# Kernel optimization log

Hardware: AMD Instinct MI355X
Metric: run time of the kernel (lower is better)

## Reference

```python
import jax, jax.numpy as jnp
import numpy as np
import math

B, LQ, LK, D, H = 4, 1024, 1024, 1024, 16
DK = D // H
SCALE = 1.0 / math.sqrt(DK)
NEG_INF = -1.0e9


def setup_inputs() -> dict:
    key = jax.random.key(0)
    ks = jax.random.split(key, 18)
    w = lambda k: (jax.random.normal(k, (D, D), dtype=jnp.float32) * 0.02)
    b = lambda k: (jax.random.normal(k, (D,), dtype=jnp.float32) * 0.02)
    mask = jax.random.randint(ks[4], (B, 1, LK), 0, 2).astype(jnp.int32)
    mask = mask.at[..., 0].set(1)  # ensure at least one valid key per row
    return {
        "query": jax.random.normal(ks[0], (B, LQ, D), dtype=jnp.float32),
        "key": jax.random.normal(ks[1], (B, LK, D), dtype=jnp.float32),
        "value": jax.random.normal(ks[2], (B, LK, D), dtype=jnp.float32),
        "weak_rela": jax.random.normal(ks[3], (B, LK, D), dtype=jnp.float32),
        "mask": mask,
        "Wq": w(ks[5]), "bq": b(ks[6]),
        "Wk": w(ks[7]), "bk": b(ks[8]),
        "Wv": w(ks[9]), "bv": b(ks[10]),
        "Wrk": w(ks[11]), "brk": b(ks[12]),
        "Wrv": w(ks[13]), "brv": b(ks[14]),
        "Wo": w(ks[15]), "bo": b(ks[16]),
    }


def _proj(x, W, bias):
    # x: [B, L, D] -> [B, H, L, DK]; torch Linear: y = x @ W.T + b
    y = x @ W.T + bias
    Bn, L, _ = y.shape
    return y.reshape(Bn, L, H, DK).transpose(0, 2, 1, 3)


def reference(query, key, value, weak_rela, mask,
              Wq, bq, Wk, bk, Wv, bv, Wrk, brk, Wrv, brv, Wo, bo):
    q = _proj(query, Wq, bq)        # [B,H,LQ,DK]
    k = _proj(key, Wk, bk)          # [B,H,LK,DK]
    v = _proj(value, Wv, bv)        # [B,H,LK,DK]
    rk = _proj(weak_rela, Wrk, brk) # [B,H,LK,DK]
    rv = _proj(weak_rela, Wrv, brv) # [B,H,LK,DK]

    qk = jnp.einsum('bhqd,bhkd->bhqk', q, k) * SCALE
    qr = jnp.einsum('bhqd,bhkd->bhqk', q, rk) * SCALE

    m = (mask[:, None, :, :] == 0)  # [B,1,1,LK] broadcast over heads/queries
    qk = jnp.where(m, NEG_INF, qk)
    qr = jnp.where(m, NEG_INF, qr)

    p_vis = jax.nn.softmax(qk, axis=-1)
    p_rel = jax.nn.softmax(qr, axis=-1)

    x = (jnp.einsum('bhqk,bhkd->bhqd', p_vis, v)
         + jnp.einsum('bhqk,bhkd->bhqd', p_rel, rv))  # [B,H,LQ,DK]
    x = x.transpose(0, 2, 1, 3).reshape(query.shape[0], -1, H * DK)
    return x @ Wo.T + bo
```

## Files before the change

kernel.cpp:

```cpp
#include <hip/hip_runtime.h>
#include <stdint.h>

#define NB 4
#define NH 16
#define DKH 64
#define DMODEL 1024
#define SEQ 1024
#define SCALE 0.125f
#define NEG_INF -1.0e9f
#define K2E 0.18033688011112042f

typedef __bf16 bf16_t;
typedef __bf16 bf16x8 __attribute__((ext_vector_type(8)));
typedef __bf16 bf16x4v __attribute__((ext_vector_type(4)));
typedef float f32x4 __attribute__((ext_vector_type(4)));

typedef const uint32_t __attribute__((address_space(1)))* gas_ptr;
typedef uint32_t __attribute__((address_space(3)))* las_ptr;

__device__ __forceinline__ void gload_lds16(const void* g, void* l) {
  __builtin_amdgcn_global_load_lds((gas_ptr)g, (las_ptr)l, 16, 0, 0);
}


__global__ void cvt_multi(const float* __restrict__ i0, const float* __restrict__ i1,
                          const float* __restrict__ i2, const float* __restrict__ i3,
                          const float* __restrict__ i4, const float* __restrict__ i5,
                          bf16_t* o0, bf16_t* o1, bf16_t* o2, bf16_t* o3, bf16_t* o4, bf16_t* o5,
                          int n) {
  const int t = blockIdx.y;
  const float* in = (t == 0) ? i0 : (t == 1) ? i1 : (t == 2) ? i2 : (t == 3) ? i3 : (t == 4) ? i4 : i5;
  bf16_t* out = (t == 0) ? o0 : (t == 1) ? o1 : (t == 2) ? o2 : (t == 3) ? o3 : (t == 4) ? o4 : o5;
  const int idx = (blockIdx.x * 256 + threadIdx.x) * 4;
  if (idx >= n) return;
  const float4 v = *(const float4*)(in + idx);
  bf16x4v p;
  p[0] = (bf16_t)v.x; p[1] = (bf16_t)v.y; p[2] = (bf16_t)v.z; p[3] = (bf16_t)v.w;
  *(bf16x4v*)(out + idx) = p;
}

#define NXE ((size_t)NB * SEQ * DMODEL)
#define NWE ((size_t)DMODEL * DMODEL)

template<int MODE>
__device__ __forceinline__ void gemm128_body(
    const bf16_t* __restrict__ A, const bf16_t* __restrict__ W,
    const float* __restrict__ bias, void* __restrict__ outp,
    int m0, int n0, bf16_t* As, bf16_t* Bs) {
  const int tid = threadIdx.x;
  const int lane = tid & 63;
  const int w = tid >> 6;
  const int wm = w >> 1, wn = w & 1;
  const int g = lane >> 4, c = lane & 15;
  const int lrow = lane >> 3;
  const int lcol = ((lane & 7) * 8) ^ ((lane >> 3) << 3);
  const int sc = (c & 7) << 3;

  f32x4 acc[4][4] = {};

  for (int kt = 0; kt < DMODEL; kt += 64) {
#pragma unroll
    for (int p = 0; p < 4; ++p) {
      const int row = w * 32 + p * 8;
      gload_lds16(A + (size_t)(m0 + row + lrow) * DMODEL + kt + lcol, &As[row * 64]);
      gload_lds16(W + (size_t)(n0 + row + lrow) * DMODEL + kt + lcol, &Bs[row * 64]);
    }
    __syncthreads();
    bf16x8 af[4][2], bfr[4][2];
#pragma unroll
    for (int i = 0; i < 4; ++i)
#pragma unroll
      for (int kk = 0; kk < 2; ++kk) {
        af[i][kk]  = *(const bf16x8*)&As[(wm * 64 + i * 16 + c) * 64 + ((kk * 32 + g * 8) ^ sc)];
        bfr[i][kk] = *(const bf16x8*)&Bs[(wn * 64 + i * 16 + c) * 64 + ((kk * 32 + g * 8) ^ sc)];
      }
#pragma unroll
    for (int i = 0; i < 4; ++i)
#pragma unroll
      for (int j = 0; j < 4; ++j) {
        acc[i][j] = __builtin_amdgcn_mfma_f32_16x16x32_bf16(af[i][0], bfr[j][0], acc[i][j], 0, 0, 0);
        acc[i][j] = __builtin_amdgcn_mfma_f32_16x16x32_bf16(af[i][1], bfr[j][1], acc[i][j], 0, 0, 0);
      }
    __syncthreads();
  }

  float bv4[4];
#pragma unroll
  for (int j = 0; j < 4; ++j) bv4[j] = bias[n0 + wn * 64 + j * 16 + c];

#pragma unroll
  for (int i = 0; i < 4; ++i) {
    const int mrow = m0 + wm * 64 + i * 16 + g * 4;
    const int b_ = mrow >> 10, l_ = mrow & 1023;
#pragma unroll
    for (int j = 0; j < 4; ++j) {
      const int n = n0 + wn * 64 + j * 16 + c;
      if (MODE == 2) {
        float* o = (float*)outp;
#pragma unroll
        for (int r = 0; r < 4; ++r)
          o[(size_t)(mrow + r) * DMODEL + n] = acc[i][j][r] + bv4[j];
      } else if (MODE == 0) {
        bf16_t* o = (bf16_t*)outp;
        const int h_ = n >> 6, dk_ = n & 63;
#pragma unroll
        for (int r = 0; r < 4; ++r)
          o[((size_t)(b_ * NH + h_) * SEQ + l_ + r) * DKH + dk_] =
              (bf16_t)(acc[i][j][r] + bv4[j]);
      } else {
        bf16_t* o = (bf16_t*)outp;
        const int h_ = n >> 6, dk_ = n & 63;
        bf16x4v pk;
#pragma unroll
        for (int r = 0; r < 4; ++r) pk[r] = (bf16_t)(acc[i][j][r] + bv4[j]);
        *(bf16x4v*)&o[((size_t)(b_ * NH + h_) * DKH + dk_) * SEQ + l_] = pk;
      }
    }
  }
}

__global__ void __launch_bounds__(256, 2)
proj_gemm(const bf16_t* __restrict__ Xbase, const bf16_t* __restrict__ Wbase,
          bf16_t* __restrict__ Obase,
          const float* __restrict__ b0, const float* __restrict__ b1,
          const float* __restrict__ b2, const float* __restrict__ b3,
          const float* __restrict__ b4) {
  __shared__ bf16_t As[128 * 64];
  __shared__ bf16_t Bs[128 * 64];
  const int bid = blockIdx.x;
  const int lid = (bid & 7) * 160 + (bid >> 3);
  const int seg = lid >> 8;
  const int rr = lid & 255;
  const int m0 = (rr >> 3) * 128, n0 = (rr & 7) * 128;

  const bf16_t* A = Xbase + (size_t)((seg < 3) ? seg : 3) * NXE;
  const bf16_t* W = Wbase + (size_t)seg * NWE;
  const int ooff = (seg == 0) ? 0 : (seg == 1) ? 1 : (seg == 2) ? 3 : (seg == 3) ? 2 : 4;
  bf16_t* out = Obase + (size_t)ooff * NXE;
  const float* bias = (seg == 0) ? b0 : (seg == 1) ? b1 : (seg == 2) ? b2 : (seg == 3) ? b3 : b4;

  if (seg == 2 || seg == 4) gemm128_body<1>(A, W, bias, out, m0, n0, As, Bs);
  else                      gemm128_body<0>(A, W, bias, out, m0, n0, As, Bs);
}

__global__ void __launch_bounds__(256, 2)
out_gemm(const bf16_t* __restrict__ A, const bf16_t* __restrict__ W,
         const float* __restrict__ bias, float* __restrict__ out) {
  __shared__ bf16_t As[128 * 64];
  __shared__ bf16_t Bs[128 * 64];
  const int bid = blockIdx.x;
  const int lid = (bid & 7) * 32 + (bid >> 3);
  const int m0 = (lid >> 3) * 128, n0 = (lid & 7) * 128;
  gemm128_body<2>(A, W, bias, out, m0, n0, As, Bs);
}

__device__ __forceinline__ void attn_step(
    const bf16_t* __restrict__ Kt, const bf16_t* __restrict__ Vt,
    bf16_t* __restrict__ Pw, const bf16x8 (&qf)[2][2], const int4 (&mk)[4],
    float (&m_s)[2], float (&l_s)[2], f32x4 (&o_s)[2][4], int lane) {
  const int g = lane >> 4, c = lane & 15;
  const int sc = (c & 7) << 3;

  f32x4 s[2][4];
  {
    bf16x8 kfr[4][2];
#pragma unroll
    for (int f = 0; f < 4; ++f) {
      kfr[f][0] = *(const bf16x8*)&Kt[(f * 16 + c) * 64 + ((g * 8) ^ sc)];
      kfr[f][1] = *(const bf16x8*)&Kt[(f * 16 + c) * 64 + ((32 + g * 8) ^ sc)];
    }
#pragma unroll
    for (int i = 0; i < 2; ++i)
#pragma unroll
      for (int f = 0; f < 4; ++f) {
        f32x4 a = {0.f, 0.f, 0.f, 0.f};
        a = __builtin_amdgcn_mfma_f32_16x16x32_bf16(kfr[f][0], qf[i][0], a, 0, 0, 0);
        a = __builtin_amdgcn_mfma_f32_16x16x32_bf16(kfr[f][1], qf[i][1], a, 0, 0, 0);
        s[i][f] = a;
      }
  }

#pragma unroll
  for (int i = 0; i < 2; ++i)
#pragma unroll
    for (int f = 0; f < 4; ++f) {
      const int4 m4 = mk[f];
      s[i][f][0] = (m4.x == 0) ? NEG_INF : s[i][f][0] * K2E;
      s[i][f][1] = (m4.y == 0) ? NEG_INF : s[i][f][1] * K2E;
      s[i][f][2] = (m4.z == 0) ? NEG_INF : s[i][f][2] * K2E;
      s[i][f][3] = (m4.w == 0) ? NEG_INF : s[i][f][3] * K2E;
    }

#pragma unroll
  for (int i = 0; i < 2; ++i) {
    float tm = fmaxf(fmaxf(s[i][0][0], s[i][0][1]), fmaxf(s[i][0][2], s[i][0][3]));
#pragma unroll
    for (int f = 1; f < 4; ++f)
      tm = fmaxf(tm, fmaxf(fmaxf(s[i][f][0], s[i][f][1]), fmaxf(s[i][f][2], s[i][f][3])));
    tm = fmaxf(tm, __shfl_xor(tm, 16));
    tm = fmaxf(tm, __shfl_xor(tm, 32));
    const float mnew = fmaxf(m_s[i], tm);
    const float sf = __builtin_amdgcn_exp2f(m_s[i] - mnew);
    m_s[i] = mnew;
    float pf = 0.f;
#pragma unroll
    for (int f = 0; f < 4; ++f) {
      bf16x4v pk;
#pragma unroll
      for (int r = 0; r < 4; ++r) {
        const float p = __builtin_amdgcn_exp2f(s[i][f][r] - mnew);
        pf += p;
        pk[r] = (bf16_t)p;
      }
      *(bf16x4v*)&Pw[i * 1024 + c * 64 + ((f * 16 + g * 4) ^ sc)] = pk;
    }
    l_s[i] = l_s[i] * sf + pf;
#pragma unroll
    for (int jd = 0; jd < 4; ++jd)
#pragma unroll
      for (int r = 0; r < 4; ++r) o_s[i][jd][r] *= sf;
  }

  bf16x8 pa[2][2];
#pragma unroll
  for (int i = 0; i < 2; ++i) {
    pa[i][0] = *(const bf16x8*)&Pw[i * 1024 + c * 64 + ((g * 8) ^ sc)];
    pa[i][1] = *(const bf16x8*)&Pw[i * 1024 + c * 64 + ((32 + g * 8) ^ sc)];
  }
#pragma unroll
  for (int jd = 0; jd < 4; ++jd) {
    const bf16x8 v0 = *(const bf16x8*)&Vt[(jd * 16 + c) * 64 + ((g * 8) ^ sc)];
    const bf16x8 v1 = *(const bf16x8*)&Vt[(jd * 16 + c) * 64 + ((32 + g * 8) ^ sc)];
#pragma unroll
    for (int i = 0; i < 2; ++i) {
      o_s[i][jd] = __builtin_amdgcn_mfma_f32_16x16x32_bf16(v0, pa[i][0], o_s[i][jd], 0, 0, 0);
      o_s[i][jd] = __builtin_amdgcn_mfma_f32_16x16x32_bf16(v1, pa[i][1], o_s[i][jd], 0, 0, 0);
    }
  }
}

__global__ void __launch_bounds__(256, 2)
attn_kernel(const bf16_t* __restrict__ q, const bf16_t* __restrict__ k,
            const bf16_t* __restrict__ rk, const bf16_t* __restrict__ vT,
            const bf16_t* __restrict__ rvT, const int* __restrict__ mask,
            bf16_t* __restrict__ x) {
  __shared__ bf16_t Ks[64 * 64], RKs[64 * 64], Vs[64 * 64], RVs[64 * 64];
  __shared__ bf16_t Ps[4][2][16 * 64];

  const int tid = threadIdx.x;
  const int lane = tid & 63;
  const int w = tid >> 6;
  const int g = lane >> 4, c = lane & 15;
  const int bid = blockIdx.x;
  const int lid = (bid & 7) * 64 + (bid >> 3);
  const int qt = lid & 7;
  const int bh = lid >> 3;
  const int b = bh >> 4, h = bh & 15;
  const int q0 = qt * 128;

  const bf16_t* qp = q + (size_t)bh * SEQ * DKH;
  const bf16_t* kp = k + (size_t)bh * SEQ * DKH;
  const bf16_t* rkp = rk + (size_t)bh * SEQ * DKH;
  const bf16_t* vp = vT + (size_t)bh * DKH * SEQ;
  const bf16_t* rvp = rvT + (size_t)bh * DKH * SEQ;
  const int* mp = mask + b * SEQ;
  const int lrow = lane >> 3;
  const int lcol = ((lane & 7) * 8) ^ ((lane >> 3) << 3);

  bf16x8 qf[2][2];
#pragma unroll
  for (int i = 0; i < 2; ++i)
#pragma unroll
    for (int kk = 0; kk < 2; ++kk)
      qf[i][kk] = *(const bf16x8*)(qp + (size_t)(q0 + w * 32 + i * 16 + c) * DKH + kk * 32 + g * 8);

  f32x4 ov[2][4] = {}, orl[2][4] = {};
  float mv[2] = {NEG_INF, NEG_INF}, mr[2] = {NEG_INF, NEG_INF};
  float lv[2] = {0.f, 0.f}, lr[2] = {0.f, 0.f};

  for (int t = 0; t < 16; ++t) {
    const int kv0 = t * 64;
    if (t) __syncthreads();
#pragma unroll
    for (int p = 0; p < 2; ++p) {
      const int row = w * 16 + p * 8;
      gload_lds16(kp  + (size_t)(kv0 + row + lrow) * DKH + lcol, &Ks[row * 64]);
      gload_lds16(rkp + (size_t)(kv0 + row + lrow) * DKH + lcol, &RKs[row * 64]);
      gload_lds16(vp  + (size_t)(row + lrow) * SEQ + kv0 + lcol, &Vs[row * 64]);
      gload_lds16(rvp + (size_t)(row + lrow) * SEQ + kv0 + lcol, &RVs[row * 64]);
    }
    __syncthreads();

    int4 mk4[4];
#pragma unroll
    for (int f = 0; f < 4; ++f) mk4[f] = *(const int4*)&mp[kv0 + f * 16 + g * 4];

    attn_step(Ks,  Vs,  &Ps[w][0][0], qf, mk4, mv, lv, ov,  lane);
    attn_step(RKs, RVs, &Ps[w][0][0], qf, mk4, mr, lr, orl, lane);
  }

#pragma unroll
  for (int i = 0; i < 2; ++i) {
    lv[i] += __shfl_xor(lv[i], 16); lv[i] += __shfl_xor(lv[i], 32);
    lr[i] += __shfl_xor(lr[i], 16); lr[i] += __shfl_xor(lr[i], 32);
  }

  bf16_t* xb = x + (size_t)b * SEQ * DMODEL + (size_t)h * DKH;
#pragma unroll
  for (int i = 0; i < 2; ++i) {
    const float rlv = 1.0f / lv[i], rlr = 1.0f / lr[i];
    const int qrow = q0 + w * 32 + i * 16 + c;
#pragma unroll
    for (int jd = 0; jd < 4; ++jd) {
      bf16x4v pk;
#pragma unroll
      for (int r = 0; r < 4; ++r)
        pk[r] = (bf16_t)(ov[i][jd][r] * rlv + orl[i][jd][r] * rlr);
      *(bf16x4v*)&xb[(size_t)qrow * DMODEL + jd * 16 + g * 4] = pk;
    }
  }
}

extern "C" void kernel_launch(void* const* d_in, const int* in_sizes, int n_in,
                              void* d_out, int out_size, void* d_ws, size_t ws_size,
                              hipStream_t stream) {
  (void)in_sizes; (void)n_in; (void)out_size; (void)ws_size;
  const float* query = (const float*)d_in[0];
  const float* key_  = (const float*)d_in[1];
  const float* value = (const float*)d_in[2];
  const float* weak  = (const float*)d_in[3];
  const int*   mask  = (const int*)d_in[4];
  const float* Wq  = (const float*)d_in[5];  const float* bq  = (const float*)d_in[6];
  const float* Wk  = (const float*)d_in[7];  const float* bk  = (const float*)d_in[8];
  const float* Wv  = (const float*)d_in[9];  const float* bv  = (const float*)d_in[10];
  const float* Wrk = (const float*)d_in[11]; const float* brk = (const float*)d_in[12];
  const float* Wrv = (const float*)d_in[13]; const float* brv = (const float*)d_in[14];
  const float* Wo  = (const float*)d_in[15]; const float* bo  = (const float*)d_in[16];

  char* ws = (char*)d_ws;
  size_t off = 0;
  auto alloc = [&](size_t bytes) {
    void* p = ws + off;
    off += (bytes + 255) & ~(size_t)255;
    return p;
  };
  const size_t SZ_X = NXE * sizeof(bf16_t);
  const size_t SZ_W = NWE * sizeof(bf16_t);

  bf16_t* Xq = (bf16_t*)alloc(SZ_X);
  bf16_t* Xk = (bf16_t*)alloc(SZ_X);
  bf16_t* Xv = (bf16_t*)alloc(SZ_X);
  bf16_t* Xr = (bf16_t*)alloc(SZ_X);
  bf16_t* Wqb  = (bf16_t*)alloc(SZ_W);
  bf16_t* Wkb  = (bf16_t*)alloc(SZ_W);
  bf16_t* Wvb  = (bf16_t*)alloc(SZ_W);
  bf16_t* Wrkb = (bf16_t*)alloc(SZ_W);
  bf16_t* Wrvb = (bf16_t*)alloc(SZ_W);
  bf16_t* Wob  = (bf16_t*)alloc(SZ_W);
  bf16_t* qh   = (bf16_t*)alloc(SZ_X);
  bf16_t* kh   = (bf16_t*)alloc(SZ_X);
  bf16_t* rkh  = (bf16_t*)alloc(SZ_X);
  bf16_t* vTh  = (bf16_t*)alloc(SZ_X);
  bf16_t* rvTh = (bf16_t*)alloc(SZ_X);
  bf16_t* xh   = (bf16_t*)alloc(SZ_X);
  (void)Xk; (void)Xv; (void)Xr; (void)Wkb; (void)Wvb; (void)Wrkb; (void)Wrvb;
  (void)kh; (void)rkh; (void)vTh; (void)rvTh;

  cvt_multi<<<dim3(4096, 4), 256, 0, stream>>>(query, key_, value, weak, nullptr, nullptr,
                                               Xq, Xk, Xv, Xr, nullptr, nullptr,
                                               NB * SEQ * DMODEL);
  cvt_multi<<<dim3(1024, 6), 256, 0, stream>>>(Wq, Wk, Wv, Wrk, Wrv, Wo,
                                               Wqb, Wkb, Wvb, Wrkb, Wrvb, Wob,
                                               DMODEL * DMODEL);

  proj_gemm<<<dim3(1280), 256, 0, stream>>>(Xq, Wqb, qh, bq, bk, bv, brk, brv);

  attn_kernel<<<dim3(512), 256, 0, stream>>>(qh, kh, rkh, vTh, rvTh, mask, xh);

  out_gemm<<<dim3(256), 256, 0, stream>>>(xh, Wob, bo, (float*)d_out);
}
```

Measured before the change: 170.4 us.

## Split attention into separate visual and relation branches across blocks, merge afterwards

Each attention block now handles only one of the two softmax branches (visual or relation), doubling the grid to 1024 blocks and halving per-block LDS and register state. Occupancy hint rises to 3 blocks per CU. Each branch writes normalized fp32 partial outputs into reused workspace buffers, and a new merge kernel sums them and converts to bf16 for the output GEMM. The trade is more parallelism against extra global traffic: fp32 intermediates written and read back, plus one more launch.

```diff
diff --git a/kernel.cpp b/kernel.cpp
--- a/kernel.cpp
+++ b/kernel.cpp
@@ -39,6 +39,18 @@
   *(bf16x4v*)(out + idx) = p;
 }
 
+__global__ void merge_x(const float* __restrict__ xv, const float* __restrict__ xr,
+                        bf16_t* __restrict__ xh, int n) {
+  const int idx = (blockIdx.x * 256 + threadIdx.x) * 4;
+  if (idx >= n) return;
+  const float4 a = *(const float4*)(xv + idx);
+  const float4 b = *(const float4*)(xr + idx);
+  bf16x4v p;
+  p[0] = (bf16_t)(a.x + b.x); p[1] = (bf16_t)(a.y + b.y);
+  p[2] = (bf16_t)(a.z + b.z); p[3] = (bf16_t)(a.w + b.w);
+  *(bf16x4v*)(xh + idx) = p;
+}
+
 #define NXE ((size_t)NB * SEQ * DMODEL)
 #define NWE ((size_t)DMODEL * DMODEL)
 
@@ -154,115 +166,32 @@
   gemm128_body<2>(A, W, bias, out, m0, n0, As, Bs);
 }
 
-__device__ __forceinline__ void attn_step(
-    const bf16_t* __restrict__ Kt, const bf16_t* __restrict__ Vt,
-    bf16_t* __restrict__ Pw, const bf16x8 (&qf)[2][2], const int4 (&mk)[4],
-    float (&m_s)[2], float (&l_s)[2], f32x4 (&o_s)[2][4], int lane) {
-  const int g = lane >> 4, c = lane & 15;
-  const int sc = (c & 7) << 3;
-
-  f32x4 s[2][4];
-  {
-    bf16x8 kfr[4][2];
-#pragma unroll
-    for (int f = 0; f < 4; ++f) {
-      kfr[f][0] = *(const bf16x8*)&Kt[(f * 16 + c) * 64 + ((g * 8) ^ sc)];
-      kfr[f][1] = *(const bf16x8*)&Kt[(f * 16 + c) * 64 + ((32 + g * 8) ^ sc)];
-    }
-#pragma unroll
-    for (int i = 0; i < 2; ++i)
-#pragma unroll
-      for (int f = 0; f < 4; ++f) {
-        f32x4 a = {0.f, 0.f, 0.f, 0.f};
-        a = __builtin_amdgcn_mfma_f32_16x16x32_bf16(kfr[f][0], qf[i][0], a, 0, 0, 0);
-        a = __builtin_amdgcn_mfma_f32_16x16x32_bf16(kfr[f][1], qf[i][1], a, 0, 0, 0);
-        s[i][f] = a;
-      }
-  }
-
-#pragma unroll
-  for (int i = 0; i < 2; ++i)
-#pragma unroll
-    for (int f = 0; f < 4; ++f) {
-      const int4 m4 = mk[f];
-      s[i][f][0] = (m4.x == 0) ? NEG_INF : s[i][f][0] * K2E;
-      s[i][f][1] = (m4.y == 0) ? NEG_INF : s[i][f][1] * K2E;
-      s[i][f][2] = (m4.z == 0) ? NEG_INF : s[i][f][2] * K2E;
-      s[i][f][3] = (m4.w == 0) ? NEG_INF : s[i][f][3] * K2E;
-    }
-
-#pragma unroll
-  for (int i = 0; i < 2; ++i) {
-    float tm = fmaxf(fmaxf(s[i][0][0], s[i][0][1]), fmaxf(s[i][0][2], s[i][0][3]));
-#pragma unroll
-    for (int f = 1; f < 4; ++f)
-      tm = fmaxf(tm, fmaxf(fmaxf(s[i][f][0], s[i][f][1]), fmaxf(s[i][f][2], s[i][f][3])));
-    tm = fmaxf(tm, __shfl_xor(tm, 16));
-    tm = fmaxf(tm, __shfl_xor(tm, 32));
-    const float mnew = fmaxf(m_s[i], tm);
-    const float sf = __builtin_amdgcn_exp2f(m_s[i] - mnew);
-    m_s[i] = mnew;
-    float pf = 0.f;
-#pragma unroll
-    for (int f = 0; f < 4; ++f) {
-      bf16x4v pk;
-#pragma unroll
-      for (int r = 0; r < 4; ++r) {
-        const float p = __builtin_amdgcn_exp2f(s[i][f][r] - mnew);
-        pf += p;
-        pk[r] = (bf16_t)p;
-      }
-      *(bf16x4v*)&Pw[i * 1024 + c * 64 + ((f * 16 + g * 4) ^ sc)] = pk;
-    }
-    l_s[i] = l_s[i] * sf + pf;
-#pragma unroll
-    for (int jd = 0; jd < 4; ++jd)
-#pragma unroll
-      for (int r = 0; r < 4; ++r) o_s[i][jd][r] *= sf;
-  }
-
-  bf16x8 pa[2][2];
-#pragma unroll
-  for (int i = 0; i < 2; ++i) {
-    pa[i][0] = *(const bf16x8*)&Pw[i * 1024 + c * 64 + ((g * 8) ^ sc)];
-    pa[i][1] = *(const bf16x8*)&Pw[i * 1024 + c * 64 + ((32 + g * 8) ^ sc)];
-  }
-#pragma unroll
-  for (int jd = 0; jd < 4; ++jd) {
-    const bf16x8 v0 = *(const bf16x8*)&Vt[(jd * 16 + c) * 64 + ((g * 8) ^ sc)];
-    const bf16x8 v1 = *(const bf16x8*)&Vt[(jd * 16 + c) * 64 + ((32 + g * 8) ^ sc)];
-#pragma unroll
-    for (int i = 0; i < 2; ++i) {
-      o_s[i][jd] = __builtin_amdgcn_mfma_f32_16x16x32_bf16(v0, pa[i][0], o_s[i][jd], 0, 0, 0);
-      o_s[i][jd] = __builtin_amdgcn_mfma_f32_16x16x32_bf16(v1, pa[i][1], o_s[i][jd], 0, 0, 0);
-    }
-  }
-}
-
-__global__ void __launch_bounds__(256, 2)
+__global__ void __launch_bounds__(256, 3)
 attn_kernel(const bf16_t* __restrict__ q, const bf16_t* __restrict__ k,
             const bf16_t* __restrict__ rk, const bf16_t* __restrict__ vT,
             const bf16_t* __restrict__ rvT, const int* __restrict__ mask,
-            bf16_t* __restrict__ x) {
-  __shared__ bf16_t Ks[64 * 64], RKs[64 * 64], Vs[64 * 64], RVs[64 * 64];
+            float* __restrict__ xv, float* __restrict__ xr) {
+  __shared__ bf16_t Ks[64 * 64], Vs[64 * 64];
   __shared__ bf16_t Ps[4][2][16 * 64];
 
   const int tid = threadIdx.x;
   const int lane = tid & 63;
   const int w = tid >> 6;
   const int g = lane >> 4, c = lane & 15;
+  const int sc = (c & 7) << 3;
   const int bid = blockIdx.x;
-  const int lid = (bid & 7) * 64 + (bid >> 3);
-  const int qt = lid & 7;
-  const int bh = lid >> 3;
+  const int lid = (bid & 7) * 128 + (bid >> 3);
+  const int br = lid >> 9;
+  const int rem = lid & 511;
+  const int qt = rem & 7;
+  const int bh = rem >> 3;
   const int b = bh >> 4, h = bh & 15;
   const int q0 = qt * 128;
 
   const bf16_t* qp = q + (size_t)bh * SEQ * DKH;
-  const bf16_t* kp = k + (size_t)bh * SEQ * DKH;
-  const bf16_t* rkp = rk + (size_t)bh * SEQ * DKH;
-  const bf16_t* vp = vT + (size_t)bh * DKH * SEQ;
-  const bf16_t* rvp = rvT + (size_t)bh * DKH * SEQ;
+  const bf16_t* kp = (br ? rk : k) + (size_t)bh * SEQ * DKH;
+  const bf16_t* vp = (br ? rvT : vT) + (size_t)bh * DKH * SEQ;
+  float* xp = br ? xr : xv;
   const int* mp = mask + b * SEQ;
   const int lrow = lane >> 3;
   const int lcol = ((lane & 7) * 8) ^ ((lane >> 3) << 3);
@@ -274,9 +203,10 @@
     for (int kk = 0; kk < 2; ++kk)
       qf[i][kk] = *(const bf16x8*)(qp + (size_t)(q0 + w * 32 + i * 16 + c) * DKH + kk * 32 + g * 8);
 
-  f32x4 ov[2][4] = {}, orl[2][4] = {};
-  float mv[2] = {NEG_INF, NEG_INF}, mr[2] = {NEG_INF, NEG_INF};
-  float lv[2] = {0.f, 0.f}, lr[2] = {0.f, 0.f};
+  f32x4 ov[2][4] = {};
+  float mv[2] = {NEG_INF, NEG_INF};
+  float lv[2] = {0.f, 0.f};
+  bf16_t* Pw = &Ps[w][0][0];
 
   for (int t = 0; t < 16; ++t) {
     const int kv0 = t * 64;
@@ -284,10 +214,8 @@
 #pragma unroll
     for (int p = 0; p < 2; ++p) {
       const int row = w * 16 + p * 8;
-      gload_lds16(kp  + (size_t)(kv0 + row + lrow) * DKH + lcol, &Ks[row * 64]);
-      gload_lds16(rkp + (size_t)(kv0 + row + lrow) * DKH + lcol, &RKs[row * 64]);
-      gload_lds16(vp  + (size_t)(row + lrow) * SEQ + kv0 + lcol, &Vs[row * 64]);
-      gload_lds16(rvp + (size_t)(row + lrow) * SEQ + kv0 + lcol, &RVs[row * 64]);
+      gload_lds16(kp + (size_t)(kv0 + row + lrow) * DKH + lcol, &Ks[row * 64]);
+      gload_lds16(vp + (size_t)(row + lrow) * SEQ + kv0 + lcol, &Vs[row * 64]);
     }
     __syncthreads();
 
@@ -295,28 +223,100 @@
 #pragma unroll
     for (int f = 0; f < 4; ++f) mk4[f] = *(const int4*)&mp[kv0 + f * 16 + g * 4];
 
-    attn_step(Ks,  Vs,  &Ps[w][0][0], qf, mk4, mv, lv, ov,  lane);
-    attn_step(RKs, RVs, &Ps[w][0][0], qf, mk4, mr, lr, orl, lane);
+    f32x4 s[2][4];
+    {
+      bf16x8 kfr[4][2];
+#pragma unroll
+      for (int f = 0; f < 4; ++f) {
+        kfr[f][0] = *(const bf16x8*)&Ks[(f * 16 + c) * 64 + ((g * 8) ^ sc)];
+        kfr[f][1] = *(const bf16x8*)&Ks[(f * 16 + c) * 64 + ((32 + g * 8) ^ sc)];
+      }
+#pragma unroll
+      for (int i = 0; i < 2; ++i)
+#pragma unroll
+        for (int f = 0; f < 4; ++f) {
+          f32x4 a = {0.f, 0.f, 0.f, 0.f};
+          a = __builtin_amdgcn_mfma_f32_16x16x32_bf16(kfr[f][0], qf[i][0], a, 0, 0, 0);
+          a = __builtin_amdgcn_mfma_f32_16x16x32_bf16(kfr[f][1], qf[i][1], a, 0, 0, 0);
+          s[i][f] = a;
+        }
+    }
+
+#pragma unroll
+    for (int i = 0; i < 2; ++i)
+#pragma unroll
+      for (int f = 0; f < 4; ++f) {
+        const int4 m4 = mk4[f];
+        s[i][f][0] = (m4.x == 0) ? NEG_INF : s[i][f][0] * K2E;
+        s[i][f][1] = (m4.y == 0) ? NEG_INF : s[i][f][1] * K2E;
+        s[i][f][2] = (m4.z == 0) ? NEG_INF : s[i][f][2] * K2E;
+        s[i][f][3] = (m4.w == 0) ? NEG_INF : s[i][f][3] * K2E;
+      }
+
+#pragma unroll
+    for (int i = 0; i < 2; ++i) {
+      float tm = fmaxf(fmaxf(s[i][0][0], s[i][0][1]), fmaxf(s[i][0][2], s[i][0][3]));
+#pragma unroll
+      for (int f = 1; f < 4; ++f)
+        tm = fmaxf(tm, fmaxf(fmaxf(s[i][f][0], s[i][f][1]), fmaxf(s[i][f][2], s[i][f][3])));
+      tm = fmaxf(tm, __shfl_xor(tm, 16));
+      tm = fmaxf(tm, __shfl_xor(tm, 32));
+      const float mnew = fmaxf(mv[i], tm);
+      const float sf = __builtin_amdgcn_exp2f(mv[i] - mnew);
+      mv[i] = mnew;
+      float pf = 0.f;
+#pragma unroll
+      for (int f = 0; f < 4; ++f) {
+        bf16x4v pk;
+#pragma unroll
+        for (int r = 0; r < 4; ++r) {
+          const float p = __builtin_amdgcn_exp2f(s[i][f][r] - mnew);
+          pf += p;
+          pk[r] = (bf16_t)p;
+        }
+        *(bf16x4v*)&Pw[i * 1024 + c * 64 + ((f * 16 + g * 4) ^ sc)] = pk;
+      }
+      lv[i] = lv[i] * sf + pf;
+#pragma unroll
+      for (int jd = 0; jd < 4; ++jd)
+#pragma unroll
+        for (int r = 0; r < 4; ++r) ov[i][jd][r] *= sf;
+    }
+
+    bf16x8 pa[2][2];
+#pragma unroll
+    for (int i = 0; i < 2; ++i) {
+      pa[i][0] = *(const bf16x8*)&Pw[i * 1024 + c * 64 + ((g * 8) ^ sc)];
+      pa[i][1] = *(const bf16x8*)&Pw[i * 1024 + c * 64 + ((32 + g * 8) ^ sc)];
+    }
+#pragma unroll
+    for (int jd = 0; jd < 4; ++jd) {
+      const bf16x8 v0 = *(const bf16x8*)&Vs[(jd * 16 + c) * 64 + ((g * 8) ^ sc)];
+      const bf16x8 v1 = *(const bf16x8*)&Vs[(jd * 16 + c) * 64 + ((32 + g * 8) ^ sc)];
+#pragma unroll
+      for (int i = 0; i < 2; ++i) {
+        ov[i][jd] = __builtin_amdgcn_mfma_f32_16x16x32_bf16(v0, pa[i][0], ov[i][jd], 0, 0, 0);
+        ov[i][jd] = __builtin_amdgcn_mfma_f32_16x16x32_bf16(v1, pa[i][1], ov[i][jd], 0, 0, 0);
+      }
+    }
   }
 
 #pragma unroll
   for (int i = 0; i < 2; ++i) {
     lv[i] += __shfl_xor(lv[i], 16); lv[i] += __shfl_xor(lv[i], 32);
-    lr[i] += __shfl_xor(lr[i], 16); lr[i] += __shfl_xor(lr[i], 32);
-  }
-
-  bf16_t* xb = x + (size_t)b * SEQ * DMODEL + (size_t)h * DKH;
+  }
+
 #pragma unroll
   for (int i = 0; i < 2; ++i) {
-    const float rlv = 1.0f / lv[i], rlr = 1.0f / lr[i];
+    const float rl = 1.0f / lv[i];
     const int qrow = q0 + w * 32 + i * 16 + c;
+    float* xrow = xp + (size_t)(b * SEQ + qrow) * DMODEL + h * DKH;
 #pragma unroll
     for (int jd = 0; jd < 4; ++jd) {
-      bf16x4v pk;
-#pragma unroll
-      for (int r = 0; r < 4; ++r)
-        pk[r] = (bf16_t)(ov[i][jd][r] * rlv + orl[i][jd][r] * rlr);
-      *(bf16x4v*)&xb[(size_t)qrow * DMODEL + jd * 16 + g * 4] = pk;
+      f32x4 st;
+#pragma unroll
+      for (int r = 0; r < 4; ++r) st[r] = ov[i][jd][r] * rl;
+      *(f32x4*)&xrow[jd * 16 + g * 4] = st;
     }
   }
 }
@@ -366,6 +366,9 @@
   (void)Xk; (void)Xv; (void)Xr; (void)Wkb; (void)Wvb; (void)Wrkb; (void)Wrvb;
   (void)kh; (void)rkh; (void)vTh; (void)rvTh;
 
+  float* xv = (float*)Xq;
+  float* xrp = (float*)Xv;
+
   cvt_multi<<<dim3(4096, 4), 256, 0, stream>>>(query, key_, value, weak, nullptr, nullptr,
                                                Xq, Xk, Xv, Xr, nullptr, nullptr,
                                                NB * SEQ * DMODEL);
@@ -375,7 +378,9 @@
 
   proj_gemm<<<dim3(1280), 256, 0, stream>>>(Xq, Wqb, qh, bq, bk, bv, brk, brv);
 
-  attn_kernel<<<dim3(512), 256, 0, stream>>>(qh, kh, rkh, vTh, rvTh, mask, xh);
+  attn_kernel<<<dim3(1024), 256, 0, stream>>>(qh, kh, rkh, vTh, rvTh, mask, xv, xrp);
+
+  merge_x<<<dim3(4096), 256, 0, stream>>>(xv, xrp, xh, (int)NXE);
 
   out_gemm<<<dim3(256), 256, 0, stream>>>(xh, Wob, bo, (float*)d_out);
 }
```

Measured after the change: 181.7 us. 1.07x slower.

## Double-buffer K tiles, precompute additive mask, and defer softmax rescaling

Applied to the files above, without the earlier changes.

Restructures the attention main loop. K tiles are double-buffered and prefetched one step ahead, and the V/RK/RV loads are issued after the K fragments are read, so the first QK^T MFMAs overlap with global-to-LDS traffic. The integer mask is turned once into an additive float bias in LDS, replacing per-element selects with a fused multiply-add. The online-softmax rescale of the accumulators is skipped unless the running max grows by more than a threshold (lazy rescaling), at some risk of larger exponent range in bf16 P values; LDS use also grows, which may affect occupancy.

```diff
diff --git a/kernel.cpp b/kernel.cpp
--- a/kernel.cpp
+++ b/kernel.cpp
@@ -154,103 +154,21 @@
   gemm128_body<2>(A, W, bias, out, m0, n0, As, Bs);
 }
 
-__device__ __forceinline__ void attn_step(
-    const bf16_t* __restrict__ Kt, const bf16_t* __restrict__ Vt,
-    bf16_t* __restrict__ Pw, const bf16x8 (&qf)[2][2], const int4 (&mk)[4],
-    float (&m_s)[2], float (&l_s)[2], f32x4 (&o_s)[2][4], int lane) {
-  const int g = lane >> 4, c = lane & 15;
-  const int sc = (c & 7) << 3;
-
-  f32x4 s[2][4];
-  {
-    bf16x8 kfr[4][2];
-#pragma unroll
-    for (int f = 0; f < 4; ++f) {
-      kfr[f][0] = *(const bf16x8*)&Kt[(f * 16 + c) * 64 + ((g * 8) ^ sc)];
-      kfr[f][1] = *(const bf16x8*)&Kt[(f * 16 + c) * 64 + ((32 + g * 8) ^ sc)];
-    }
-#pragma unroll
-    for (int i = 0; i < 2; ++i)
-#pragma unroll
-      for (int f = 0; f < 4; ++f) {
-        f32x4 a = {0.f, 0.f, 0.f, 0.f};
-        a = __builtin_amdgcn_mfma_f32_16x16x32_bf16(kfr[f][0], qf[i][0], a, 0, 0, 0);
-        a = __builtin_amdgcn_mfma_f32_16x16x32_bf16(kfr[f][1], qf[i][1], a, 0, 0, 0);
-        s[i][f] = a;
-      }
-  }
-
-#pragma unroll
-  for (int i = 0; i < 2; ++i)
-#pragma unroll
-    for (int f = 0; f < 4; ++f) {
-      const int4 m4 = mk[f];
-      s[i][f][0] = (m4.x == 0) ? NEG_INF : s[i][f][0] * K2E;
-      s[i][f][1] = (m4.y == 0) ? NEG_INF : s[i][f][1] * K2E;
-      s[i][f][2] = (m4.z == 0) ? NEG_INF : s[i][f][2] * K2E;
-      s[i][f][3] = (m4.w == 0) ? NEG_INF : s[i][f][3] * K2E;
-    }
-
-#pragma unroll
-  for (int i = 0; i < 2; ++i) {
-    float tm = fmaxf(fmaxf(s[i][0][0], s[i][0][1]), fmaxf(s[i][0][2], s[i][0][3]));
-#pragma unroll
-    for (int f = 1; f < 4; ++f)
-      tm = fmaxf(tm, fmaxf(fmaxf(s[i][f][0], s[i][f][1]), fmaxf(s[i][f][2], s[i][f][3])));
-    tm = fmaxf(tm, __shfl_xor(tm, 16));
-    tm = fmaxf(tm, __shfl_xor(tm, 32));
-    const float mnew = fmaxf(m_s[i], tm);
-    const float sf = __builtin_amdgcn_exp2f(m_s[i] - mnew);
-    m_s[i] = mnew;
-    float pf = 0.f;
-#pragma unroll
-    for (int f = 0; f < 4; ++f) {
-      bf16x4v pk;
-#pragma unroll
-      for (int r = 0; r < 4; ++r) {
-        const float p = __builtin_amdgcn_exp2f(s[i][f][r] - mnew);
-        pf += p;
-        pk[r] = (bf16_t)p;
-      }
-      *(bf16x4v*)&Pw[i * 1024 + c * 64 + ((f * 16 + g * 4) ^ sc)] = pk;
-    }
-    l_s[i] = l_s[i] * sf + pf;
-#pragma unroll
-    for (int jd = 0; jd < 4; ++jd)
-#pragma unroll
-      for (int r = 0; r < 4; ++r) o_s[i][jd][r] *= sf;
-  }
-
-  bf16x8 pa[2][2];
-#pragma unroll
-  for (int i = 0; i < 2; ++i) {
-    pa[i][0] = *(const bf16x8*)&Pw[i * 1024 + c * 64 + ((g * 8) ^ sc)];
-    pa[i][1] = *(const bf16x8*)&Pw[i * 1024 + c * 64 + ((32 + g * 8) ^ sc)];
-  }
-#pragma unroll
-  for (int jd = 0; jd < 4; ++jd) {
-    const bf16x8 v0 = *(const bf16x8*)&Vt[(jd * 16 + c) * 64 + ((g * 8) ^ sc)];
-    const bf16x8 v1 = *(const bf16x8*)&Vt[(jd * 16 + c) * 64 + ((32 + g * 8) ^ sc)];
-#pragma unroll
-    for (int i = 0; i < 2; ++i) {
-      o_s[i][jd] = __builtin_amdgcn_mfma_f32_16x16x32_bf16(v0, pa[i][0], o_s[i][jd], 0, 0, 0);
-      o_s[i][jd] = __builtin_amdgcn_mfma_f32_16x16x32_bf16(v1, pa[i][1], o_s[i][jd], 0, 0, 0);
-    }
-  }
-}
-
 __global__ void __launch_bounds__(256, 2)
 attn_kernel(const bf16_t* __restrict__ q, const bf16_t* __restrict__ k,
             const bf16_t* __restrict__ rk, const bf16_t* __restrict__ vT,
             const bf16_t* __restrict__ rvT, const int* __restrict__ mask,
             bf16_t* __restrict__ x) {
-  __shared__ bf16_t Ks[64 * 64], RKs[64 * 64], Vs[64 * 64], RVs[64 * 64];
+  __shared__ bf16_t Ks0[64 * 64], Ks1[64 * 64];
+  __shared__ bf16_t RKs[64 * 64], Vs[64 * 64], RVs[64 * 64];
   __shared__ bf16_t Ps[4][2][16 * 64];
+  __shared__ float Mb[SEQ];
 
   const int tid = threadIdx.x;
   const int lane = tid & 63;
   const int w = tid >> 6;
   const int g = lane >> 4, c = lane & 15;
+  const int sc = (c & 7) << 3;
   const int bid = blockIdx.x;
   const int lid = (bid & 7) * 64 + (bid >> 3);
   const int qt = lid & 7;
@@ -266,7 +184,18 @@
   const int* mp = mask + b * SEQ;
   const int lrow = lane >> 3;
   const int lcol = ((lane & 7) * 8) ^ ((lane >> 3) << 3);
-
+  bf16_t* Pw = &Ps[w][0][0];
+
+#pragma unroll
+  for (int p = 0; p < 2; ++p) {
+    const int row = w * 16 + p * 8;
+    gload_lds16(kp + (size_t)(row + lrow) * DKH + lcol, &Ks0[row * 64]);
+  }
+#pragma unroll
+  for (int i = 0; i < 4; ++i) {
+    const int idx = i * 256 + tid;
+    Mb[idx] = (mp[idx] == 0) ? NEG_INF : 0.0f;
+  }
   bf16x8 qf[2][2];
 #pragma unroll
   for (int i = 0; i < 2; ++i)
@@ -278,25 +207,186 @@
   float mv[2] = {NEG_INF, NEG_INF}, mr[2] = {NEG_INF, NEG_INF};
   float lv[2] = {0.f, 0.f}, lr[2] = {0.f, 0.f};
 
-  for (int t = 0; t < 16; ++t) {
+  __syncthreads();
+
+  auto step = [&](int t, const bf16_t* KC, bf16_t* KN) {
     const int kv0 = t * 64;
-    if (t) __syncthreads();
+
+    bf16x8 kfr[4][2];
+#pragma unroll
+    for (int f = 0; f < 4; ++f) {
+      kfr[f][0] = *(const bf16x8*)&KC[(f * 16 + c) * 64 + ((g * 8) ^ sc)];
+      kfr[f][1] = *(const bf16x8*)&KC[(f * 16 + c) * 64 + ((32 + g * 8) ^ sc)];
+    }
+
 #pragma unroll
     for (int p = 0; p < 2; ++p) {
       const int row = w * 16 + p * 8;
-      gload_lds16(kp  + (size_t)(kv0 + row + lrow) * DKH + lcol, &Ks[row * 64]);
-      gload_lds16(rkp + (size_t)(kv0 + row + lrow) * DKH + lcol, &RKs[row * 64]);
       gload_lds16(vp  + (size_t)(row + lrow) * SEQ + kv0 + lcol, &Vs[row * 64]);
       gload_lds16(rvp + (size_t)(row + lrow) * SEQ + kv0 + lcol, &RVs[row * 64]);
-    }
+      gload_lds16(rkp + (size_t)(kv0 + row + lrow) * DKH + lcol, &RKs[row * 64]);
+    }
+    if (t < 15) {
+#pragma unroll
+      for (int p = 0; p < 2; ++p) {
+        const int row = w * 16 + p * 8;
+        gload_lds16(kp + (size_t)(kv0 + 64 + row + lrow) * DKH + lcol, &KN[row * 64]);
+      }
+    }
+
+    f32x4 mb[4];
+#pragma unroll
+    for (int f = 0; f < 4; ++f)
+      mb[f] = *(const f32x4*)&Mb[kv0 + f * 16 + g * 4];
+
+    f32x4 s[2][4];
+#pragma unroll
+    for (int i = 0; i < 2; ++i)
+#pragma unroll
+      for (int f = 0; f < 4; ++f) {
+        f32x4 a = {0.f, 0.f, 0.f, 0.f};
+        a = __builtin_amdgcn_mfma_f32_16x16x32_bf16(kfr[f][0], qf[i][0], a, 0, 0, 0);
+        a = __builtin_amdgcn_mfma_f32_16x16x32_bf16(kfr[f][1], qf[i][1], a, 0, 0, 0);
+        s[i][f] = a;
+      }
+
+#pragma unroll
+    for (int i = 0; i < 2; ++i) {
+#pragma unroll
+      for (int f = 0; f < 4; ++f)
+#pragma unroll
+        for (int r = 0; r < 4; ++r)
+          s[i][f][r] = s[i][f][r] * K2E + mb[f][r];
+      float tm = fmaxf(fmaxf(s[i][0][0], s[i][0][1]), fmaxf(s[i][0][2], s[i][0][3]));
+#pragma unroll
+      for (int f = 1; f < 4; ++f)
+        tm = fmaxf(tm, fmaxf(fmaxf(s[i][f][0], s[i][f][1]), fmaxf(s[i][f][2], s[i][f][3])));
+      tm = fmaxf(tm, __shfl_xor(tm, 16));
+      tm = fmaxf(tm, __shfl_xor(tm, 32));
+      if (!__all(tm <= mv[i] + 8.0f)) {
+        const float mnew = fmaxf(mv[i], tm);
+        const float sf = __builtin_amdgcn_exp2f(mv[i] - mnew);
+        mv[i] = mnew;
+        lv[i] *= sf;
+#pragma unroll
+        for (int jd = 0; jd < 4; ++jd)
+#pragma unroll
+          for (int r = 0; r < 4; ++r) ov[i][jd][r] *= sf;
+      }
+      float pf = 0.f;
+#pragma unroll
+      for (int f = 0; f < 4; ++f) {
+        bf16x4v pk;
+#pragma unroll
+        for (int r = 0; r < 4; ++r) {
+          const float p = __builtin_amdgcn_exp2f(s[i][f][r] - mv[i]);
+          pf += p;
+          pk[r] = (bf16_t)p;
+        }
+        *(bf16x4v*)&Pw[i * 1024 + c * 64 + ((f * 16 + g * 4) ^ sc)] = pk;
+      }
+      lv[i] += pf;
+    }
+
     __syncthreads();
 
-    int4 mk4[4];
-#pragma unroll
-    for (int f = 0; f < 4; ++f) mk4[f] = *(const int4*)&mp[kv0 + f * 16 + g * 4];
-
-    attn_step(Ks,  Vs,  &Ps[w][0][0], qf, mk4, mv, lv, ov,  lane);
-    attn_step(RKs, RVs, &Ps[w][0][0], qf, mk4, mr, lr, orl, lane);
+    {
+      bf16x8 pa[2][2];
+#pragma unroll
+      for (int i = 0; i < 2; ++i) {
+        pa[i][0] = *(const bf16x8*)&Pw[i * 1024 + c * 64 + ((g * 8) ^ sc)];
+        pa[i][1] = *(const bf16x8*)&Pw[i * 1024 + c * 64 + ((32 + g * 8) ^ sc)];
+      }
+#pragma unroll
+      for (int jd = 0; jd < 4; ++jd) {
+        const bf16x8 v0 = *(const bf16x8*)&Vs[(jd * 16 + c) * 64 + ((g * 8) ^ sc)];
+        const bf16x8 v1 = *(const bf16x8*)&Vs[(jd * 16 + c) * 64 + ((32 + g * 8) ^ sc)];
+#pragma unroll
+        for (int i = 0; i < 2; ++i) {
+          ov[i][jd] = __builtin_amdgcn_mfma_f32_16x16x32_bf16(v0, pa[i][0], ov[i][jd], 0, 0, 0);
+          ov[i][jd] = __builtin_amdgcn_mfma_f32_16x16x32_bf16(v1, pa[i][1], ov[i][jd], 0, 0, 0);
+        }
+      }
+    }
+
+#pragma unroll
+    for (int f = 0; f < 4; ++f) {
+      kfr[f][0] = *(const bf16x8*)&RKs[(f * 16 + c) * 64 + ((g * 8) ^ sc)];
+      kfr[f][1] = *(const bf16x8*)&RKs[(f * 16 + c) * 64 + ((32 + g * 8) ^ sc)];
+    }
+#pragma unroll
+    for (int i = 0; i < 2; ++i)
+#pragma unroll
+      for (int f = 0; f < 4; ++f) {
+        f32x4 a = {0.f, 0.f, 0.f, 0.f};
+        a = __builtin_amdgcn_mfma_f32_16x16x32_bf16(kfr[f][0], qf[i][0], a, 0, 0, 0);
+        a = __builtin_amdgcn_mfma_f32_16x16x32_bf16(kfr[f][1], qf[i][1], a, 0, 0, 0);
+        s[i][f] = a;
+      }
+
+#pragma unroll
+    for (int i = 0; i < 2; ++i) {
+#pragma unroll
+      for (int f = 0; f < 4; ++f)
+#pragma unroll
+        for (int r = 0; r < 4; ++r)
+          s[i][f][r] = s[i][f][r] * K2E + mb[f][r];
+      float tm = fmaxf(fmaxf(s[i][0][0], s[i][0][1]), fmaxf(s[i][0][2], s[i][0][3]));
+#pragma unroll
+      for (int f = 1; f < 4; ++f)
+        tm = fmaxf(tm, fmaxf(fmaxf(s[i][f][0], s[i][f][1]), fmaxf(s[i][f][2], s[i][f][3])));
+      tm = fmaxf(tm, __shfl_xor(tm, 16));
+      tm = fmaxf(tm, __shfl_xor(tm, 32));
+      if (!__all(tm <= mr[i] + 8.0f)) {
+        const float mnew = fmaxf(mr[i], tm);
+        const float sf = __builtin_amdgcn_exp2f(mr[i] - mnew);
+        mr[i] = mnew;
+        lr[i] *= sf;
+#pragma unroll
+        for (int jd = 0; jd < 4; ++jd)
+#pragma unroll
+          for (int r = 0; r < 4; ++r) orl[i][jd][r] *= sf;
+      }
+      float pf = 0.f;
+#pragma unroll
+      for (int f = 0; f < 4; ++f) {
+        bf16x4v pk;
+#pragma unroll
+        for (int r = 0; r < 4; ++r) {
+          const float p = __builtin_amdgcn_exp2f(s[i][f][r] - mr[i]);
+          pf += p;
+          pk[r] = (bf16_t)p;
+        }
+        *(bf16x4v*)&Pw[i * 1024 + c * 64 + ((f * 16 + g * 4) ^ sc)] = pk;
+      }
+      lr[i] += pf;
+    }
+
+    {
+      bf16x8 pa[2][2];
+#pragma unroll
+      for (int i = 0; i < 2; ++i) {
+        pa[i][0] = *(const bf16x8*)&Pw[i * 1024 + c * 64 + ((g * 8) ^ sc)];
+        pa[i][1] = *(const bf16x8*)&Pw[i * 1024 + c * 64 + ((32 + g * 8) ^ sc)];
+      }
+#pragma unroll
+      for (int jd = 0; jd < 4; ++jd) {
+        const bf16x8 v0 = *(const bf16x8*)&RVs[(jd * 16 + c) * 64 + ((g * 8) ^ sc)];
+        const bf16x8 v1 = *(const bf16x8*)&RVs[(jd * 16 + c) * 64 + ((32 + g * 8) ^ sc)];
+#pragma unroll
+        for (int i = 0; i < 2; ++i) {
+          orl[i][jd] = __builtin_amdgcn_mfma_f32_16x16x32_bf16(v0, pa[i][0], orl[i][jd], 0, 0, 0);
+          orl[i][jd] = __builtin_amdgcn_mfma_f32_16x16x32_bf16(v1, pa[i][1], orl[i][jd], 0, 0, 0);
+        }
+      }
+    }
+
+    __syncthreads();
+  };
+
+  for (int tt = 0; tt < 8; ++tt) {
+    step(tt * 2,     Ks0, Ks1);
+    step(tt * 2 + 1, Ks1, Ks0);
   }
 
 #pragma unroll
```

After: 172.5 us. Within noise of the previous version (+1.3%).

## Switch attention to 32x32x16 MFMA with register-resident P via permlane swap

Applied to the files above, without the earlier changes.

Rewrites the attention inner step to use 32x32x16 bf16 MFMA tiles instead of 16x16x32. The probability matrix is now packed with v_cvt_pk_bf16 and rearranged across lanes with v_permlane32_swap, so it no longer round-trips through LDS; the per-wave P scratch buffer is removed. The goal is fewer LDS writes and reads, fewer MFMA issues and fewer cross-lane reductions. In exchange, register pressure rises from the larger f32x16 accumulators, and the fragment-layout mapping is delicate to get right.

```diff
diff --git a/kernel.cpp b/kernel.cpp
--- a/kernel.cpp
+++ b/kernel.cpp
@@ -14,12 +14,30 @@
 typedef __bf16 bf16x8 __attribute__((ext_vector_type(8)));
 typedef __bf16 bf16x4v __attribute__((ext_vector_type(4)));
 typedef float f32x4 __attribute__((ext_vector_type(4)));
+typedef float f32x16 __attribute__((ext_vector_type(16)));
+typedef uint32_t u32x4 __attribute__((ext_vector_type(4)));
 
 typedef const uint32_t __attribute__((address_space(1)))* gas_ptr;
 typedef uint32_t __attribute__((address_space(3)))* las_ptr;
 
 __device__ __forceinline__ void gload_lds16(const void* g, void* l) {
   __builtin_amdgcn_global_load_lds((gas_ptr)g, (las_ptr)l, 16, 0, 0);
+}
+
+__device__ __forceinline__ f32x16 z16() {
+  f32x16 v;
+#pragma unroll
+  for (int i = 0; i < 16; ++i) v[i] = 0.f;
+  return v;
+}
+
+__device__ __forceinline__ uint32_t cvtpk_bf16(float lo, float hi) {
+  uint32_t r;
+  asm("v_cvt_pk_bf16_f32 %0, %1, %2" : "=v"(r) : "v"(lo), "v"(hi));
+  return r;
+}
+__device__ __forceinline__ void plane32_swap(uint32_t& a, uint32_t& b) {
+  asm("v_permlane32_swap_b32 %0, %1" : "+v"(a), "+v"(b));
 }
 
 
@@ -154,88 +172,82 @@
   gemm128_body<2>(A, W, bias, out, m0, n0, As, Bs);
 }
 
-__device__ __forceinline__ void attn_step(
+__device__ __forceinline__ void attn_branch(
     const bf16_t* __restrict__ Kt, const bf16_t* __restrict__ Vt,
-    bf16_t* __restrict__ Pw, const bf16x8 (&qf)[2][2], const int4 (&mk)[4],
-    float (&m_s)[2], float (&l_s)[2], f32x4 (&o_s)[2][4], int lane) {
-  const int g = lane >> 4, c = lane & 15;
-  const int sc = (c & 7) << 3;
-
-  f32x4 s[2][4];
-  {
-    bf16x8 kfr[4][2];
-#pragma unroll
-    for (int f = 0; f < 4; ++f) {
-      kfr[f][0] = *(const bf16x8*)&Kt[(f * 16 + c) * 64 + ((g * 8) ^ sc)];
-      kfr[f][1] = *(const bf16x8*)&Kt[(f * 16 + c) * 64 + ((32 + g * 8) ^ sc)];
-    }
-#pragma unroll
-    for (int i = 0; i < 2; ++i)
-#pragma unroll
-      for (int f = 0; f < 4; ++f) {
-        f32x4 a = {0.f, 0.f, 0.f, 0.f};
-        a = __builtin_amdgcn_mfma_f32_16x16x32_bf16(kfr[f][0], qf[i][0], a, 0, 0, 0);
-        a = __builtin_amdgcn_mfma_f32_16x16x32_bf16(kfr[f][1], qf[i][1], a, 0, 0, 0);
-        s[i][f] = a;
-      }
-  }
-
-#pragma unroll
-  for (int i = 0; i < 2; ++i)
-#pragma unroll
-    for (int f = 0; f < 4; ++f) {
-      const int4 m4 = mk[f];
-      s[i][f][0] = (m4.x == 0) ? NEG_INF : s[i][f][0] * K2E;
-      s[i][f][1] = (m4.y == 0) ? NEG_INF : s[i][f][1] * K2E;
-      s[i][f][2] = (m4.z == 0) ? NEG_INF : s[i][f][2] * K2E;
-      s[i][f][3] = (m4.w == 0) ? NEG_INF : s[i][f][3] * K2E;
-    }
-
-#pragma unroll
-  for (int i = 0; i < 2; ++i) {
-    float tm = fmaxf(fmaxf(s[i][0][0], s[i][0][1]), fmaxf(s[i][0][2], s[i][0][3]));
-#pragma unroll
-    for (int f = 1; f < 4; ++f)
-      tm = fmaxf(tm, fmaxf(fmaxf(s[i][f][0], s[i][f][1]), fmaxf(s[i][f][2], s[i][f][3])));
-    tm = fmaxf(tm, __shfl_xor(tm, 16));
-    tm = fmaxf(tm, __shfl_xor(tm, 32));
-    const float mnew = fmaxf(m_s[i], tm);
-    const float sf = __builtin_amdgcn_exp2f(m_s[i] - mnew);
-    m_s[i] = mnew;
-    float pf = 0.f;
-#pragma unroll
-    for (int f = 0; f < 4; ++f) {
-      bf16x4v pk;
-#pragma unroll
-      for (int r = 0; r < 4; ++r) {
-        const float p = __builtin_amdgcn_exp2f(s[i][f][r] - mnew);
-        pf += p;
-        pk[r] = (bf16_t)p;
-      }
-      *(bf16x4v*)&Pw[i * 1024 + c * 64 + ((f * 16 + g * 4) ^ sc)] = pk;
-    }
-    l_s[i] = l_s[i] * sf + pf;
-#pragma unroll
-    for (int jd = 0; jd < 4; ++jd)
-#pragma unroll
-      for (int r = 0; r < 4; ++r) o_s[i][jd][r] *= sf;
-  }
-
-  bf16x8 pa[2][2];
-#pragma unroll
-  for (int i = 0; i < 2; ++i) {
-    pa[i][0] = *(const bf16x8*)&Pw[i * 1024 + c * 64 + ((g * 8) ^ sc)];
-    pa[i][1] = *(const bf16x8*)&Pw[i * 1024 + c * 64 + ((32 + g * 8) ^ sc)];
-  }
-#pragma unroll
-  for (int jd = 0; jd < 4; ++jd) {
-    const bf16x8 v0 = *(const bf16x8*)&Vt[(jd * 16 + c) * 64 + ((g * 8) ^ sc)];
-    const bf16x8 v1 = *(const bf16x8*)&Vt[(jd * 16 + c) * 64 + ((32 + g * 8) ^ sc)];
-#pragma unroll
-    for (int i = 0; i < 2; ++i) {
-      o_s[i][jd] = __builtin_amdgcn_mfma_f32_16x16x32_bf16(v0, pa[i][0], o_s[i][jd], 0, 0, 0);
-      o_s[i][jd] = __builtin_amdgcn_mfma_f32_16x16x32_bf16(v1, pa[i][1], o_s[i][jd], 0, 0, 0);
-    }
+    const bf16x8 (&qB)[4], const int4 (&mk)[2][4],
+    float& m_s, float& l_s, f32x16& oA, f32x16& oB, int lane31, int hh, int srow) {
+  f32x16 s[2];
+#pragma unroll
+  for (int kvh = 0; kvh < 2; ++kvh) {
+    f32x16 a = z16();
+    const bf16_t* kr = &Kt[(kvh * 32 + lane31) * 64];
+#pragma unroll
+    for (int kk = 0; kk < 4; ++kk) {
+      const bf16x8 ka = *(const bf16x8*)&kr[(kk * 16 + hh * 8) ^ srow];
+      a = __builtin_amdgcn_mfma_f32_32x32x16_bf16(ka, qB[kk], a, 0, 0, 0);
+    }
+    s[kvh] = a;
+  }
+
+  float tm = NEG_INF;
+#pragma unroll
+  for (int kvh = 0; kvh < 2; ++kvh)
+#pragma unroll
+    for (int m = 0; m < 16; ++m) {
+      const int4 q4 = mk[kvh][m >> 2];
+      const int mval = ((m & 3) == 0) ? q4.x : ((m & 3) == 1) ? q4.y
+                     : ((m & 3) == 2) ? q4.z : q4.w;
+      const float v = mval ? s[kvh][m] * K2E : NEG_INF;
+      s[kvh][m] = v;
+      tm = fmaxf(tm, v);
+    }
+  tm = fmaxf(tm, __shfl_xor(tm, 32));
+
+  const float mnew = fmaxf(m_s, tm);
+  const float sf = __builtin_amdgcn_exp2f(m_s - mnew);
+  m_s = mnew;
+
+  float pf = 0.f;
+#pragma unroll
+  for (int kvh = 0; kvh < 2; ++kvh)
+#pragma unroll
+    for (int m = 0; m < 16; ++m) {
+      const float p = __builtin_amdgcn_exp2f(s[kvh][m] - mnew);
+      s[kvh][m] = p;
+      pf += p;
+    }
+  l_s = l_s * sf + pf;
+#pragma unroll
+  for (int m = 0; m < 16; ++m) { oA[m] *= sf; oB[m] *= sf; }
+
+  bf16x8 pb[4];
+#pragma unroll
+  for (int kvh = 0; kvh < 2; ++kvh) {
+    uint32_t pkA0 = cvtpk_bf16(s[kvh][0],  s[kvh][1]);
+    uint32_t pkA1 = cvtpk_bf16(s[kvh][4],  s[kvh][5]);
+    uint32_t pkB0 = cvtpk_bf16(s[kvh][2],  s[kvh][3]);
+    uint32_t pkB1 = cvtpk_bf16(s[kvh][6],  s[kvh][7]);
+    uint32_t pkA2 = cvtpk_bf16(s[kvh][8],  s[kvh][9]);
+    uint32_t pkA3 = cvtpk_bf16(s[kvh][12], s[kvh][13]);
+    uint32_t pkB2 = cvtpk_bf16(s[kvh][10], s[kvh][11]);
+    uint32_t pkB3 = cvtpk_bf16(s[kvh][14], s[kvh][15]);
+    plane32_swap(pkA0, pkA1);
+    plane32_swap(pkB0, pkB1);
+    plane32_swap(pkA2, pkA3);
+    plane32_swap(pkB2, pkB3);
+    const u32x4 w0 = {pkA0, pkB0, pkA1, pkB1};
+    const u32x4 w1 = {pkA2, pkB2, pkA3, pkB3};
+    pb[2 * kvh]     = __builtin_bit_cast(bf16x8, w0);
+    pb[2 * kvh + 1] = __builtin_bit_cast(bf16x8, w1);
+  }
+
+#pragma unroll
+  for (int s4 = 0; s4 < 4; ++s4) {
+    const int col = (s4 * 16 + hh * 8) ^ srow;
+    const bf16x8 va = *(const bf16x8*)&Vt[(lane31) * 64 + col];
+    oA = __builtin_amdgcn_mfma_f32_32x32x16_bf16(va, pb[s4], oA, 0, 0, 0);
+    const bf16x8 vb = *(const bf16x8*)&Vt[(32 + lane31) * 64 + col];
+    oB = __builtin_amdgcn_mfma_f32_32x32x16_bf16(vb, pb[s4], oB, 0, 0, 0);
   }
 }
 
@@ -245,12 +257,12 @@
             const bf16_t* __restrict__ rvT, const int* __restrict__ mask,
             bf16_t* __restrict__ x) {
   __shared__ bf16_t Ks[64 * 64], RKs[64 * 64], Vs[64 * 64], RVs[64 * 64];
-  __shared__ bf16_t Ps[4][2][16 * 64];
 
   const int tid = threadIdx.x;
   const int lane = tid & 63;
   const int w = tid >> 6;
-  const int g = lane >> 4, c = lane & 15;
+  const int lane31 = lane & 31, hh = lane >> 5;
+  const int srow = (lane31 & 7) << 3;
   const int bid = blockIdx.x;
   const int lid = (bid & 7) * 64 + (bid >> 3);
   const int qt = lid & 7;
@@ -267,16 +279,13 @@
   const int lrow = lane >> 3;
   const int lcol = ((lane & 7) * 8) ^ ((lane >> 3) << 3);
 
-  bf16x8 qf[2][2];
-#pragma unroll
-  for (int i = 0; i < 2; ++i)
-#pragma unroll
-    for (int kk = 0; kk < 2; ++kk)
-      qf[i][kk] = *(const bf16x8*)(qp + (size_t)(q0 + w * 32 + i * 16 + c) * DKH + kk * 32 + g * 8);
-
-  f32x4 ov[2][4] = {}, orl[2][4] = {};
-  float mv[2] = {NEG_INF, NEG_INF}, mr[2] = {NEG_INF, NEG_INF};
-  float lv[2] = {0.f, 0.f}, lr[2] = {0.f, 0.f};
+  bf16x8 qB[4];
+#pragma unroll
+  for (int kk = 0; kk < 4; ++kk)
+    qB[kk] = *(const bf16x8*)(qp + (size_t)(q0 + w * 32 + lane31) * DKH + kk * 16 + hh * 8);
+
+  f32x16 ov[2] = {z16(), z16()}, orr[2] = {z16(), z16()};
+  float mv = NEG_INF, mr = NEG_INF, lv = 0.f, lr = 0.f;
 
   for (int t = 0; t < 16; ++t) {
     const int kv0 = t * 64;
@@ -291,34 +300,33 @@
     }
     __syncthreads();
 
-    int4 mk4[4];
-#pragma unroll
-    for (int f = 0; f < 4; ++f) mk4[f] = *(const int4*)&mp[kv0 + f * 16 + g * 4];
-
-    attn_step(Ks,  Vs,  &Ps[w][0][0], qf, mk4, mv, lv, ov,  lane);
-    attn_step(RKs, RVs, &Ps[w][0][0], qf, mk4, mr, lr, orl, lane);
-  }
-
-#pragma unroll
-  for (int i = 0; i < 2; ++i) {
-    lv[i] += __shfl_xor(lv[i], 16); lv[i] += __shfl_xor(lv[i], 32);
-    lr[i] += __shfl_xor(lr[i], 16); lr[i] += __shfl_xor(lr[i], 32);
-  }
+    int4 mk[2][4];
+#pragma unroll
+    for (int kh = 0; kh < 2; ++kh)
+#pragma unroll
+      for (int mq = 0; mq < 4; ++mq)
+        mk[kh][mq] = *(const int4*)&mp[kv0 + kh * 32 + 8 * mq + 4 * hh];
+
+    attn_branch(Ks,  Vs,  qB, mk, mv, lv, ov[0],  ov[1],  lane31, hh, srow);
+    attn_branch(RKs, RVs, qB, mk, mr, lr, orr[0], orr[1], lane31, hh, srow);
+  }
+
+  lv += __shfl_xor(lv, 32);
+  lr += __shfl_xor(lr, 32);
+  const float rlv = 1.0f / lv, rlr = 1.0f / lr;
 
   bf16_t* xb = x + (size_t)b * SEQ * DMODEL + (size_t)h * DKH;
-#pragma unroll
-  for (int i = 0; i < 2; ++i) {
-    const float rlv = 1.0f / lv[i], rlr = 1.0f / lr[i];
-    const int qrow = q0 + w * 32 + i * 16 + c;
-#pragma unroll
-    for (int jd = 0; jd < 4; ++jd) {
+  const int qrow = q0 + w * 32 + lane31;
+#pragma unroll
+  for (int dh = 0; dh < 2; ++dh)
+#pragma unroll
+    for (int mq = 0; mq < 4; ++mq) {
       bf16x4v pk;
 #pragma unroll
       for (int r = 0; r < 4; ++r)
-        pk[r] = (bf16_t)(ov[i][jd][r] * rlv + orl[i][jd][r] * rlr);
-      *(bf16x4v*)&xb[(size_t)qrow * DMODEL + jd * 16 + g * 4] = pk;
-    }
-  }
+        pk[r] = (bf16_t)(ov[dh][4 * mq + r] * rlv + orr[dh][4 * mq + r] * rlr);
+      *(bf16x4v*)&xb[(size_t)qrow * DMODEL + dh * 32 + 8 * mq + 4 * hh] = pk;
+    }
 }
 
 extern "C" void kernel_launch(void* const* d_in, const int* in_sizes, int n_in,
```

Result: slower. 179.0 us (+5.0%).
